# Kernel tuning notes

Hardware: AMD Instinct MI355X
Metric: run time of the kernel (lower is better)

The kernel has to match this reference:

```python
import jax, jax.numpy as jnp
import numpy as np

D_MODEL = 2048
N_HEADS = 16
N_KV_HEADS = 4
D_K = D_MODEL // N_HEADS  # 128
N_REP = N_HEADS // N_KV_HEADS
WINDOW = 128  # current_window_size default
RMS_EPS = 1e-8
ROPE_BASE = 10000.0
MASK_FILL = -10000.0


def _rmsnorm(x, w):
    rms = jnp.sqrt(jnp.mean(x * x, axis=-1, keepdims=True) + RMS_EPS)
    return x / rms * w


def _rope(x, cos, sin):
    # x: [B, S, H, d_k]; cos/sin: [S, d_k//2]; pairs are interleaved (..., -1, 2)
    B, S, H, dk = x.shape
    xr = x.reshape(B, S, H, dk // 2, 2)
    x1, x2 = xr[..., 0], xr[..., 1]
    c = cos[None, :, None, :]
    s = sin[None, :, None, :]
    o1 = x1 * c - x2 * s
    o2 = x1 * s + x2 * c
    return jnp.stack([o1, o2], axis=-1).reshape(B, S, H, dk)


def setup_inputs() -> dict:
    key = jax.random.key(0)
    ks = jax.random.split(key, 10)
    B, S = 2, 2048
    std = 1.0 / np.sqrt(D_MODEL)
    inp = {
        "x": jax.random.normal(ks[0], (B, S, D_MODEL), dtype=jnp.float32),
        "Wq": jax.random.normal(ks[1], (D_MODEL, D_MODEL), dtype=jnp.float32) * std,
        "bq": jnp.zeros((D_MODEL,), dtype=jnp.float32),
        "Wk": jax.random.normal(ks[2], (N_KV_HEADS * D_K, D_MODEL), dtype=jnp.float32) * std,
        "bk": jnp.zeros((N_KV_HEADS * D_K,), dtype=jnp.float32),
        "Wv": jax.random.normal(ks[3], (N_KV_HEADS * D_K, D_MODEL), dtype=jnp.float32) * std,
        "bv": jnp.zeros((N_KV_HEADS * D_K,), dtype=jnp.float32),
        "Wo": jax.random.normal(ks[4], (D_MODEL, D_MODEL), dtype=jnp.float32) * std,
        "bo": jnp.zeros((D_MODEL,), dtype=jnp.float32),
        "qn_w": jnp.ones((D_K,), dtype=jnp.float32),
        "kn_w": jnp.ones((D_K,), dtype=jnp.float32),
        "scale": jnp.asarray(1.0 / np.sqrt(D_K), dtype=jnp.float32),
    }
    return inp


def reference(x, Wq, bq, Wk, bk, Wv, bv, Wo, bo, qn_w, kn_w, scale):
    B, S, D = x.shape
    # projections
    q = (x @ Wq.T + bq).reshape(B, S, N_HEADS, D_K)
    k = (x @ Wk.T + bk).reshape(B, S, N_KV_HEADS, D_K)
    v = (x @ Wv.T + bv).reshape(B, S, N_KV_HEADS, D_K)
    # per-head RMSNorm
    q = _rmsnorm(q, qn_w)
    k = _rmsnorm(k, kn_w)
    # RoPE
    inv_freq = 1.0 / (ROPE_BASE ** (jnp.arange(0, D_K, 2, dtype=jnp.float32) / D_K))
    t = jnp.arange(S, dtype=jnp.float32)
    freqs = t[:, None] * inv_freq[None, :]  # [S, D_K//2]
    cos, sin = jnp.cos(freqs), jnp.sin(freqs)
    q = _rope(q, cos, sin)
    k = _rope(k, cos, sin)
    # [B, H, S, d_k]
    q = q.transpose(0, 2, 1, 3)
    k = k.transpose(0, 2, 1, 3)
    v = v.transpose(0, 2, 1, 3)
    # GQA repeat (repeat_interleave on head dim)
    k = jnp.repeat(k, N_REP, axis=1)
    v = jnp.repeat(v, N_REP, axis=1)
    # dense sliding-window path (window < seq_len)
    scores = jnp.einsum("bhqd,bhkd->bhqk", q, k) * scale
    idx = jnp.arange(S)
    causal = idx[:, None] < idx[None, :]  # triu diag=1
    local = jnp.abs(idx[:, None] - idx[None, :]) > (WINDOW // 2)
    mask = causal | local
    scores = jnp.where(mask[None, None, :, :], MASK_FILL, scores)
    attn = jax.nn.softmax(scores, axis=-1)
    out = jnp.einsum("bhqk,bhkd->bhqd", attn, v)
    out = out.transpose(0, 2, 1, 3).reshape(B, S, D)
    return out @ Wo.T + bo
```

## Files before the change

### kernel.cpp

```cpp
#include <hip/hip_runtime.h>

#define BATCH 2
#define SEQ 2048
#define DMODEL 2048
#define NHEADS 16
#define NKV 4
#define DK 128
#define WINH 64
#define NQKV 3072

typedef unsigned short ushort_t;
typedef __attribute__((ext_vector_type(8))) __bf16 bf16x8;
typedef __attribute__((ext_vector_type(4))) float f32x4;

__device__ __forceinline__ float b2f(ushort_t u) {
    union { unsigned int i; float f; } v; v.i = ((unsigned int)u) << 16; return v.f;
}
__device__ __forceinline__ ushort_t f2b(float f) {
    union { float f; unsigned int i; } v; v.f = f;
    unsigned int r = v.i + 0x7FFFu + ((v.i >> 16) & 1u);
    return (ushort_t)(r >> 16);
}

__device__ __forceinline__ void gload_lds16(const ushort_t* g, ushort_t* l) {
    __builtin_amdgcn_global_load_lds(
        (__attribute__((address_space(1))) void*)(void*)const_cast<ushort_t*>(g),
        (__attribute__((address_space(3))) void*)l, 16, 0, 0);
}

__global__ __launch_bounds__(256) void cvt_bf16(
    const float* __restrict__ src, ushort_t* __restrict__ dst, int n8)
{
    int i = blockIdx.x * 256 + threadIdx.x;
    if (i >= n8) return;
    float4 a = *((const float4*)src + i * 2);
    float4 b = *((const float4*)src + i * 2 + 1);
    ushort_t o[8] = { f2b(a.x), f2b(a.y), f2b(a.z), f2b(a.w),
                      f2b(b.x), f2b(b.y), f2b(b.z), f2b(b.w) };
    *((uint4*)dst + i) = *(const uint4*)o;
}

__global__ __launch_bounds__(256) void cvt_weights(
    const float* __restrict__ Wq, const float* __restrict__ Wk,
    const float* __restrict__ Wv, const float* __restrict__ Wo,
    ushort_t* __restrict__ dst)
{
    int i = blockIdx.x * 256 + threadIdx.x;
    int row = i >> 8;
    int c8  = i & 255;
    const float* src;
    if      (row < 2048) src = Wq + (size_t)row * 2048;
    else if (row < 2560) src = Wk + (size_t)(row - 2048) * 2048;
    else if (row < 3072) src = Wv + (size_t)(row - 2560) * 2048;
    else                 src = Wo + (size_t)(row - 3072) * 2048;
    float4 a = *((const float4*)src + c8 * 2);
    float4 b = *((const float4*)src + c8 * 2 + 1);
    ushort_t o[8] = { f2b(a.x), f2b(a.y), f2b(a.z), f2b(a.w),
                      f2b(b.x), f2b(b.y), f2b(b.z), f2b(b.w) };
    *((uint4*)dst + i) = *(const uint4*)o;
}

__global__ __launch_bounds__(256) void concat_bias3(
    const float* __restrict__ bq, const float* __restrict__ bk,
    const float* __restrict__ bv, float* __restrict__ dst)
{
    int i = blockIdx.x * 256 + threadIdx.x;
    if (i < 2048) dst[i] = bq[i];
    else if (i < 2560) dst[i] = bk[i - 2048];
    else if (i < 3072) dst[i] = bv[i - 2560];
}

__global__ __launch_bounds__(256) void gemm_qkv(
    const ushort_t* __restrict__ A, const ushort_t* __restrict__ W,
    const float* __restrict__ bias, ushort_t* __restrict__ C,
    int M, int N, int K)
{
    __shared__ __attribute__((aligned(16))) ushort_t sA[8192];
    __shared__ __attribute__((aligned(16))) ushort_t sB[8192];

    const int tid  = threadIdx.x;
    const int lane = tid & 63;
    const int wave = tid >> 6;
    const int nbn  = N >> 7;

    int nwg = gridDim.x;
    int bid = blockIdx.x;
    int nb  = (nwg & 7) ? bid : ((bid & 7) * (nwg >> 3) + (bid >> 3));
    const int bm = nb / nbn;
    const int bn = nb % nbn;
    const int m0 = bm << 7, n0 = bn << 7;
    const int wm = wave >> 1, wn = wave & 1;

    f32x4 acc[4][4] = {};

    const int frow = lane & 15;
    const int kg   = lane >> 4;

    const ushort_t* gA[4]; const ushort_t* gB[4];
    ushort_t* lA[4]; ushort_t* lB[4];
#pragma unroll
    for (int j = 0; j < 4; ++j) {
        int t = wave * 4 + j;
        int c = t * 64 + lane;
        int r = c >> 3, s = c & 7;
        int ksrc = s ^ (r & 7);
        gA[j] = A + (size_t)(m0 + r) * K + ksrc * 8;
        gB[j] = W + (size_t)(n0 + r) * K + ksrc * 8;
        lA[j] = sA + t * 512;
        lB[j] = sB + t * 512;
    }

    for (int k0 = 0; k0 < K; k0 += 64) {
        if (k0) __syncthreads();
#pragma unroll
        for (int j = 0; j < 4; ++j) gload_lds16(gA[j] + k0, lA[j]);
#pragma unroll
        for (int j = 0; j < 4; ++j) gload_lds16(gB[j] + k0, lB[j]);
        __syncthreads();

        bf16x8 af[4][2], bfr[4][2];
#pragma unroll
        for (int mi = 0; mi < 4; ++mi)
#pragma unroll
            for (int kk = 0; kk < 2; ++kk) {
                int r = (wm << 6) + (mi << 4) + frow;
                int sl = (kk * 4 + kg) ^ (r & 7);
                af[mi][kk] = *(const bf16x8*)(sA + (r * 8 + sl) * 8);
            }
#pragma unroll
        for (int ni = 0; ni < 4; ++ni)
#pragma unroll
            for (int kk = 0; kk < 2; ++kk) {
                int r = (wn << 6) + (ni << 4) + frow;
                int sl = (kk * 4 + kg) ^ (r & 7);
                bfr[ni][kk] = *(const bf16x8*)(sB + (r * 8 + sl) * 8);
            }
#pragma unroll
        for (int kk = 0; kk < 2; ++kk)
#pragma unroll
            for (int mi = 0; mi < 4; ++mi)
#pragma unroll
                for (int ni = 0; ni < 4; ++ni)
                    acc[mi][ni] = __builtin_amdgcn_mfma_f32_16x16x32_bf16(
                        af[mi][kk], bfr[ni][kk], acc[mi][ni], 0, 0, 0);
    }

    const int orow = (lane >> 4) << 2;
    const int ocol = lane & 15;
#pragma unroll
    for (int ni = 0; ni < 4; ++ni) {
        int col = n0 + (wn << 6) + (ni << 4) + ocol;
        float bvf = bias[col];
#pragma unroll
        for (int mi = 0; mi < 4; ++mi) {
#pragma unroll
            for (int r = 0; r < 4; ++r) {
                int row = m0 + (wm << 6) + (mi << 4) + orow + r;
                C[(size_t)row * N + col] = f2b(acc[mi][ni][r] + bvf);
            }
        }
    }
}

__global__ __launch_bounds__(128) void rmsrope(
    ushort_t* __restrict__ qkv, const float* __restrict__ qw,
    const float* __restrict__ kw)
{
    const int d   = threadIdx.x;
    const int blk = blockIdx.x;
    const int bs  = blk / 20;
    const int hh  = blk % 20;
    const int s   = bs & 2047;

    ushort_t* p = qkv + (size_t)bs * NQKV + hh * DK;
    const float* w = (hh < NHEADS) ? qw : kw;

    float x  = b2f(p[d]);
    float ss = x * x;
#pragma unroll
    for (int off = 32; off; off >>= 1) ss += __shfl_xor(ss, off, 64);
    float s2 = __shfl_xor(ss, 0, 64);
    __shared__ float red[2];
    if ((d & 63) == 0) red[d >> 6] = ss;
    __syncthreads();
    float tot = red[0] + red[1];
    (void)s2;
    float inv = rsqrtf(tot * (1.0f / 128.0f) + 1e-8f);
    float xn  = x * inv * w[d];

    float partner = __shfl_xor(xn, 1, 64);
    float invfreq = exp2f(-(float)(d & ~1) * (13.287712379549449f / 128.0f));
    float angle   = (float)s * invfreq;
    float c = cosf(angle), sn = sinf(angle);
    float o = (d & 1) ? (partner * sn + xn * c) : (xn * c - partner * sn);
    p[d] = f2b(o);
}

__global__ __launch_bounds__(512) void gemm_out_ks(
    const ushort_t* __restrict__ A, const ushort_t* __restrict__ W,
    const float* __restrict__ bias, float* __restrict__ C,
    int M, int N, int K)
{
    __shared__ __attribute__((aligned(16))) unsigned char smem[65536];
    ushort_t* sA = (ushort_t*)smem;
    ushort_t* sB = (ushort_t*)(smem + 16384);
    float*    red = (float*)smem;

    const int tid  = threadIdx.x;
    const int lane = tid & 63;
    const int wave = tid >> 6;
    const int g    = wave >> 2;
    const int q    = wave & 3;
    const int wm   = q >> 1, wn = q & 1;
    const int nbn  = N >> 7;

    int nwg = gridDim.x;
    int bid = blockIdx.x;
    int nb  = (nwg & 7) ? bid : ((bid & 7) * (nwg >> 3) + (bid >> 3));
    const int bm = nb / nbn;
    const int bn = nb % nbn;
    const int m0 = bm << 7, n0 = bn << 7;

    f32x4 acc[4][4] = {};

    const int frow = lane & 15;
    const int kg   = lane >> 4;

    const ushort_t* gA[2]; const ushort_t* gB[2];
    ushort_t* lA[2]; ushort_t* lB[2];
#pragma unroll
    for (int j = 0; j < 2; ++j) {
        int t = wave * 2 + j;
        int c = t * 64 + lane;
        int r = c >> 3, s = c & 7;
        int ksrc = s ^ (r & 7);
        gA[j] = A + (size_t)(m0 + r) * K + ksrc * 8;
        gB[j] = W + (size_t)(n0 + r) * K + ksrc * 8;
        lA[j] = sA + t * 512;
        lB[j] = sB + t * 512;
    }

    for (int k0 = 0; k0 < K; k0 += 64) {
        if (k0) __syncthreads();
#pragma unroll
        for (int j = 0; j < 2; ++j) gload_lds16(gA[j] + k0, lA[j]);
#pragma unroll
        for (int j = 0; j < 2; ++j) gload_lds16(gB[j] + k0, lB[j]);
        __syncthreads();

        bf16x8 af[4], bfr[4];
#pragma unroll
        for (int mi = 0; mi < 4; ++mi) {
            int r = (wm << 6) + (mi << 4) + frow;
            int sl = ((g << 2) + kg) ^ (r & 7);
            af[mi] = *(const bf16x8*)(sA + (r * 8 + sl) * 8);
        }
#pragma unroll
        for (int ni = 0; ni < 4; ++ni) {
            int r = (wn << 6) + (ni << 4) + frow;
            int sl = ((g << 2) + kg) ^ (r & 7);
            bfr[ni] = *(const bf16x8*)(sB + (r * 8 + sl) * 8);
        }
#pragma unroll
        for (int mi = 0; mi < 4; ++mi)
#pragma unroll
            for (int ni = 0; ni < 4; ++ni)
                acc[mi][ni] = __builtin_amdgcn_mfma_f32_16x16x32_bf16(
                    af[mi], bfr[ni], acc[mi][ni], 0, 0, 0);
    }

    __syncthreads();
    if (g == 1) {
#pragma unroll
        for (int mi = 0; mi < 4; ++mi)
#pragma unroll
            for (int ni = 0; ni < 4; ++ni)
                *(f32x4*)(red + q * 4096 + (mi * 4 + ni) * 256 + lane * 4) =
                    acc[mi][ni];
    }
    __syncthreads();

    if (g == 0) {
        const int orow = (lane >> 4) << 2;
        const int ocol = lane & 15;
#pragma unroll
        for (int ni = 0; ni < 4; ++ni) {
            int col = n0 + (wn << 6) + (ni << 4) + ocol;
            float bvf = bias[col];
#pragma unroll
            for (int mi = 0; mi < 4; ++mi) {
                f32x4 other = *(const f32x4*)(red + q * 4096 + (mi * 4 + ni) * 256 + lane * 4);
#pragma unroll
                for (int r = 0; r < 4; ++r) {
                    int row = m0 + (wm << 6) + (mi << 4) + orow + r;
                    C[(size_t)row * N + col] = acc[mi][ni][r] + other[r] + bvf;
                }
            }
        }
    }
}

__global__ __launch_bounds__(256) void attn_mfma(
    const ushort_t* __restrict__ qkv, const float* __restrict__ scp,
    ushort_t* __restrict__ ao)
{
    __shared__ __attribute__((aligned(16))) ushort_t sK[16384];
    __shared__ __attribute__((aligned(16))) ushort_t sVT[16384];

    const int tid  = threadIdx.x;
    const int lane = tid & 63;
    const int w    = tid >> 6;
    const int c    = lane & 15;
    const int g    = lane >> 4;

    const int blk = blockIdx.x;
    const int qt  = blk & 31;
    const int h   = (blk >> 5) & 15;
    const int b   = blk >> 9;
    const int kvh = h >> 2;
    const int i0  = qt << 6;
    const int jb  = i0 - 64;
    const float scale = scp[0];

    bf16x8 aq[4];
    {
        const ushort_t* qp = qkv + ((size_t)(b * 2048 + i0 + w * 16 + c)) * NQKV
                                 + h * 128 + g * 8;
#pragma unroll
        for (int ks = 0; ks < 4; ++ks)
            aq[ks] = *(const bf16x8*)(qp + ks * 32);
    }

    const ushort_t* kvb = qkv + ((size_t)b * 2048) * NQKV + 2048 + kvh * 128;
#pragma unroll
    for (int it = 0; it < 8; ++it) {
        int idx = it * 256 + tid;
        int rr = idx >> 4, cc = idx & 15;
        int j = jb + rr; if (j < 0) j = 0;
        uint4 val = *(const uint4*)(kvb + (size_t)j * NQKV + cc * 8);
        int f2v = (rr & 15) ^ ((rr >> 3) & 15);
        *(uint4*)(sK + (rr * 16 + (cc ^ f2v)) * 8) = val;
    }
#pragma unroll
    for (int it = 0; it < 4; ++it) {
        int task = it * 256 + tid;
        int pp = task >> 4, d8 = task & 15;
        int j0 = jb + 2 * pp;     if (j0 < 0) j0 = 0;
        int j1 = jb + 2 * pp + 1; if (j1 < 0) j1 = 0;
        ushort_t e0[8]; *(uint4*)e0 = *(const uint4*)(kvb + (size_t)j0 * NQKV + 512 + d8 * 8);
        ushort_t e1[8]; *(uint4*)e1 = *(const uint4*)(kvb + (size_t)j1 * NQKV + 512 + d8 * 8);
        int cc = pp >> 2;
#pragma unroll
        for (int jj = 0; jj < 8; ++jj) {
            int rr = d8 * 8 + jj;
            int f2v = (rr & 15) ^ ((rr >> 3) & 15);
            unsigned int word = (unsigned int)e0[jj] | ((unsigned int)e1[jj] << 16);
            *(unsigned int*)(sVT + (rr * 16 + (cc ^ f2v)) * 8 + (pp & 3) * 2) = word;
        }
    }
    __syncthreads();

    f32x4 s[8] = {};
#pragma unroll
    for (int nt = 0; nt < 8; ++nt) {
        int rr = nt * 16 + c;
        int f2v = (rr & 15) ^ ((rr >> 3) & 15);
#pragma unroll
        for (int ks = 0; ks < 4; ++ks) {
            bf16x8 bk = *(const bf16x8*)(sK + (rr * 16 + ((ks * 4 + g) ^ f2v)) * 8);
            s[nt] = __builtin_amdgcn_mfma_f32_16x16x32_bf16(aq[ks], bk, s[nt], 0, 0, 0);
        }
    }

    float linv[4];
#pragma unroll
    for (int r = 0; r < 4; ++r) {
        int qb = w * 16 + g * 4 + r;
#pragma unroll
        for (int nt = 0; nt < 8; ++nt) {
            int jl = nt * 16 + c;
            bool valid = (jl >= qb) && (jl <= qb + 64) && (i0 + jl >= 64);
            s[nt][r] = valid ? s[nt][r] * scale : -1e30f;
        }
        float m = s[0][r];
#pragma unroll
        for (int nt = 1; nt < 8; ++nt) m = fmaxf(m, s[nt][r]);
#pragma unroll
        for (int off = 1; off <= 8; off <<= 1) m = fmaxf(m, __shfl_xor(m, off, 64));
        float sum = 0.f;
#pragma unroll
        for (int nt = 0; nt < 8; ++nt) {
            float e = __expf(s[nt][r] - m);
            s[nt][r] = e;
            sum += e;
        }
#pragma unroll
        for (int off = 1; off <= 8; off <<= 1) sum += __shfl_xor(sum, off, 64);
        linv[r] = 1.0f / sum;
    }

    __syncthreads();
    float* Pw = (float*)sK + w * 2048;
#pragma unroll
    for (int nt = 0; nt < 8; ++nt) {
#pragma unroll
        for (int r = 0; r < 4; ++r) {
            int q = g * 4 + r;
            int chunk = nt * 4 + (c >> 2);
            Pw[q * 128 + ((chunk ^ (q & 7)) * 4) + (c & 3)] = s[nt][r];
        }
    }

    f32x4 o[8] = {};
#pragma unroll
    for (int kt = 0; kt < 4; ++kt) {
        float pf[8];
#pragma unroll
        for (int e = 0; e < 2; ++e) {
            int chunk = kt * 8 + g * 2 + e;
            f32x4 v4 = *(const f32x4*)(Pw + c * 128 + ((chunk ^ (c & 7)) * 4));
            pf[e * 4 + 0] = v4[0]; pf[e * 4 + 1] = v4[1];
            pf[e * 4 + 2] = v4[2]; pf[e * 4 + 3] = v4[3];
        }
        ushort_t pb[8];
#pragma unroll
        for (int j = 0; j < 8; ++j) pb[j] = f2b(pf[j]);
        bf16x8 pa = *(const bf16x8*)pb;
#pragma unroll
        for (int dt = 0; dt < 8; ++dt) {
            int rr = dt * 16 + c;
            int f2v = (rr & 15) ^ ((rr >> 3) & 15);
            bf16x8 bv = *(const bf16x8*)(sVT + (rr * 16 + ((kt * 4 + g) ^ f2v)) * 8);
            o[dt] = __builtin_amdgcn_mfma_f32_16x16x32_bf16(pa, bv, o[dt], 0, 0, 0);
        }
    }

    const size_t orow0 = (size_t)(b * 2048 + i0 + w * 16);
#pragma unroll
    for (int dt = 0; dt < 8; ++dt) {
#pragma unroll
        for (int r = 0; r < 4; ++r) {
            int q = g * 4 + r;
            ao[(orow0 + q) * 2048 + h * 128 + dt * 16 + c] = f2b(o[dt][r] * linv[r]);
        }
    }
}

extern "C" void kernel_launch(void* const* d_in, const int* in_sizes, int n_in,
                              void* d_out, int out_size, void* d_ws, size_t ws_size,
                              hipStream_t stream)
{
    const float* x   = (const float*)d_in[0];
    const float* Wq  = (const float*)d_in[1];
    const float* bq  = (const float*)d_in[2];
    const float* Wk  = (const float*)d_in[3];
    const float* bk  = (const float*)d_in[4];
    const float* Wv  = (const float*)d_in[5];
    const float* bv  = (const float*)d_in[6];
    const float* Wo  = (const float*)d_in[7];
    const float* bo  = (const float*)d_in[8];
    const float* qnw = (const float*)d_in[9];
    const float* knw = (const float*)d_in[10];
    const float* scp = (const float*)d_in[11];
    float* out = (float*)d_out;

    const int M = BATCH * SEQ;
    ushort_t* xb    = (ushort_t*)d_ws;
    ushort_t* qkv0  = xb   + (size_t)M * DMODEL;
    ushort_t* Wqkvb = qkv0 + (size_t)M * NQKV;
    ushort_t* Wob   = Wqkvb + (size_t)NQKV * DMODEL;
    float*    bqkv  = (float*)(Wob + (size_t)DMODEL * DMODEL);
    ushort_t* ao    = xb;
    (void)ws_size; (void)in_sizes; (void)n_in; (void)out_size;

    cvt_bf16<<<dim3(4096), 256, 0, stream>>>(x, xb, M * DMODEL / 8);
    cvt_weights<<<dim3(5120), 256, 0, stream>>>(Wq, Wk, Wv, Wo, Wqkvb);
    concat_bias3<<<dim3(12), 256, 0, stream>>>(bq, bk, bv, bqkv);

    gemm_qkv<<<dim3((M / 128) * (NQKV / 128)), 256, 0, stream>>>(
        xb, Wqkvb, bqkv, qkv0, M, NQKV, DMODEL);
    rmsrope<<<dim3(M * (NHEADS + NKV)), 128, 0, stream>>>(qkv0, qnw, knw);
    attn_mfma<<<dim3(BATCH * NHEADS * (SEQ / 64)), 256, 0, stream>>>(qkv0, scp, ao);
    gemm_out_ks<<<dim3((M / 128) * (DMODEL / 128)), 512, 0, stream>>>(
        ao, Wob, bo, out, M, DMODEL, DMODEL);
}
```

Measured before the change: 164.5 us.

## Fuse RMSNorm+RoPE into attention loads and merge prep kernels

Removes the standalone rmsrope kernel. Per-head RMSNorm and RoPE are now applied to Q and K as they are loaded inside the attention kernel, using a cos/sin table that is precomputed once per call. The softmax scale is folded into the Q normalisation factor. The three conversion/bias kernels are merged into one prep launch that also builds the rope table. This cuts launches and a full read-modify-write pass over qkv, at the cost of recomputing K normalisation in each query-tile block that shares the same K rows.

```diff
diff --git a/kernel.cpp b/kernel.cpp
--- a/kernel.cpp
+++ b/kernel.cpp
@@ -28,46 +28,48 @@
         (__attribute__((address_space(3))) void*)l, 16, 0, 0);
 }
 
-__global__ __launch_bounds__(256) void cvt_bf16(
-    const float* __restrict__ src, ushort_t* __restrict__ dst, int n8)
+__global__ __launch_bounds__(256) void prep(
+    const float* __restrict__ x,  const float* __restrict__ Wq,
+    const float* __restrict__ Wk, const float* __restrict__ Wv,
+    const float* __restrict__ Wo, const float* __restrict__ bq,
+    const float* __restrict__ bk, const float* __restrict__ bv,
+    ushort_t* __restrict__ xb, ushort_t* __restrict__ wdst,
+    float* __restrict__ bqkv, float2* __restrict__ rtab)
 {
-    int i = blockIdx.x * 256 + threadIdx.x;
-    if (i >= n8) return;
-    float4 a = *((const float4*)src + i * 2);
-    float4 b = *((const float4*)src + i * 2 + 1);
-    ushort_t o[8] = { f2b(a.x), f2b(a.y), f2b(a.z), f2b(a.w),
-                      f2b(b.x), f2b(b.y), f2b(b.z), f2b(b.w) };
-    *((uint4*)dst + i) = *(const uint4*)o;
-}
-
-__global__ __launch_bounds__(256) void cvt_weights(
-    const float* __restrict__ Wq, const float* __restrict__ Wk,
-    const float* __restrict__ Wv, const float* __restrict__ Wo,
-    ushort_t* __restrict__ dst)
-{
-    int i = blockIdx.x * 256 + threadIdx.x;
-    int row = i >> 8;
-    int c8  = i & 255;
-    const float* src;
-    if      (row < 2048) src = Wq + (size_t)row * 2048;
-    else if (row < 2560) src = Wk + (size_t)(row - 2048) * 2048;
-    else if (row < 3072) src = Wv + (size_t)(row - 2560) * 2048;
-    else                 src = Wo + (size_t)(row - 3072) * 2048;
-    float4 a = *((const float4*)src + c8 * 2);
-    float4 b = *((const float4*)src + c8 * 2 + 1);
-    ushort_t o[8] = { f2b(a.x), f2b(a.y), f2b(a.z), f2b(a.w),
-                      f2b(b.x), f2b(b.y), f2b(b.z), f2b(b.w) };
-    *((uint4*)dst + i) = *(const uint4*)o;
-}
-
-__global__ __launch_bounds__(256) void concat_bias3(
-    const float* __restrict__ bq, const float* __restrict__ bk,
-    const float* __restrict__ bv, float* __restrict__ dst)
-{
-    int i = blockIdx.x * 256 + threadIdx.x;
-    if (i < 2048) dst[i] = bq[i];
-    else if (i < 2560) dst[i] = bk[i - 2048];
-    else if (i < 3072) dst[i] = bv[i - 2560];
+    const int blk = blockIdx.x;
+    const int tid = threadIdx.x;
+    if (blk < 4096) {
+        int i = blk * 256 + tid;
+        float4 a = *((const float4*)x + i * 2);
+        float4 b = *((const float4*)x + i * 2 + 1);
+        ushort_t o[8] = { f2b(a.x), f2b(a.y), f2b(a.z), f2b(a.w),
+                          f2b(b.x), f2b(b.y), f2b(b.z), f2b(b.w) };
+        *((uint4*)xb + i) = *(const uint4*)o;
+    } else if (blk < 9216) {
+        int i = (blk - 4096) * 256 + tid;
+        int row = i >> 8, c8 = i & 255;
+        const float* src;
+        if      (row < 2048) src = Wq + (size_t)row * 2048;
+        else if (row < 2560) src = Wk + (size_t)(row - 2048) * 2048;
+        else if (row < 3072) src = Wv + (size_t)(row - 2560) * 2048;
+        else                 src = Wo + (size_t)(row - 3072) * 2048;
+        float4 a = *((const float4*)src + c8 * 2);
+        float4 b = *((const float4*)src + c8 * 2 + 1);
+        ushort_t o[8] = { f2b(a.x), f2b(a.y), f2b(a.z), f2b(a.w),
+                          f2b(b.x), f2b(b.y), f2b(b.z), f2b(b.w) };
+        *((uint4*)wdst + i) = *(const uint4*)o;
+    } else if (blk < 9228) {
+        int i = (blk - 9216) * 256 + tid;
+        if (i < 2048) bqkv[i] = bq[i];
+        else if (i < 2560) bqkv[i] = bk[i - 2048];
+        else if (i < 3072) bqkv[i] = bv[i - 2560];
+    } else {
+        int i = (blk - 9228) * 256 + tid;
+        int s = i >> 6, dd = i & 63;
+        float invfreq = exp2f(-(float)(2 * dd) * (13.287712379549449f / 128.0f));
+        float ang = (float)s * invfreq;
+        rtab[i] = make_float2(cosf(ang), sinf(ang));
+    }
 }
 
 __global__ __launch_bounds__(256) void gemm_qkv(
@@ -162,40 +164,6 @@
     }
 }
 
-__global__ __launch_bounds__(128) void rmsrope(
-    ushort_t* __restrict__ qkv, const float* __restrict__ qw,
-    const float* __restrict__ kw)
-{
-    const int d   = threadIdx.x;
-    const int blk = blockIdx.x;
-    const int bs  = blk / 20;
-    const int hh  = blk % 20;
-    const int s   = bs & 2047;
-
-    ushort_t* p = qkv + (size_t)bs * NQKV + hh * DK;
-    const float* w = (hh < NHEADS) ? qw : kw;
-
-    float x  = b2f(p[d]);
-    float ss = x * x;
-#pragma unroll
-    for (int off = 32; off; off >>= 1) ss += __shfl_xor(ss, off, 64);
-    float s2 = __shfl_xor(ss, 0, 64);
-    __shared__ float red[2];
-    if ((d & 63) == 0) red[d >> 6] = ss;
-    __syncthreads();
-    float tot = red[0] + red[1];
-    (void)s2;
-    float inv = rsqrtf(tot * (1.0f / 128.0f) + 1e-8f);
-    float xn  = x * inv * w[d];
-
-    float partner = __shfl_xor(xn, 1, 64);
-    float invfreq = exp2f(-(float)(d & ~1) * (13.287712379549449f / 128.0f));
-    float angle   = (float)s * invfreq;
-    float c = cosf(angle), sn = sinf(angle);
-    float o = (d & 1) ? (partner * sn + xn * c) : (xn * c - partner * sn);
-    p[d] = f2b(o);
-}
-
 __global__ __launch_bounds__(512) void gemm_out_ks(
     const ushort_t* __restrict__ A, const ushort_t* __restrict__ W,
     const float* __restrict__ bias, float* __restrict__ C,
@@ -301,8 +269,9 @@
 }
 
 __global__ __launch_bounds__(256) void attn_mfma(
-    const ushort_t* __restrict__ qkv, const float* __restrict__ scp,
-    ushort_t* __restrict__ ao)
+    const ushort_t* __restrict__ qkv, const float* __restrict__ qn_w,
+    const float* __restrict__ kn_w, const float* __restrict__ scp,
+    const float2* __restrict__ rtab, ushort_t* __restrict__ ao)
 {
     __shared__ __attribute__((aligned(16))) ushort_t sK[16384];
     __shared__ __attribute__((aligned(16))) ushort_t sVT[16384];
@@ -324,11 +293,40 @@
 
     bf16x8 aq[4];
     {
-        const ushort_t* qp = qkv + ((size_t)(b * 2048 + i0 + w * 16 + c)) * NQKV
+        const int srow = i0 + w * 16 + c;
+        const ushort_t* qp = qkv + ((size_t)(b * 2048 + srow)) * NQKV
                                  + h * 128 + g * 8;
-#pragma unroll
-        for (int ks = 0; ks < 4; ++ks)
-            aq[ks] = *(const bf16x8*)(qp + ks * 32);
+        float xv[4][8];
+        float ss = 0.f;
+#pragma unroll
+        for (int ks = 0; ks < 4; ++ks) {
+            ushort_t raw[8];
+            *(uint4*)raw = *(const uint4*)(qp + ks * 32);
+#pragma unroll
+            for (int j = 0; j < 8; ++j) {
+                float xf = b2f(raw[j]);
+                xv[ks][j] = xf;
+                ss += xf * xf;
+            }
+        }
+        ss += __shfl_xor(ss, 16, 64);
+        ss += __shfl_xor(ss, 32, 64);
+        float inv = rsqrtf(ss * (1.0f / 128.0f) + 1e-8f) * scale;
+#pragma unroll
+        for (int ks = 0; ks < 4; ++ks) {
+            ushort_t outb[8];
+#pragma unroll
+            for (int jj = 0; jj < 4; ++jj) {
+                int d = ks * 32 + g * 8 + 2 * jj;
+                float2 w2 = *(const float2*)(qn_w + d);
+                float x0 = xv[ks][2 * jj]     * inv * w2.x;
+                float x1 = xv[ks][2 * jj + 1] * inv * w2.y;
+                float2 cs = rtab[(srow << 6) + (d >> 1)];
+                outb[2 * jj]     = f2b(x0 * cs.x - x1 * cs.y);
+                outb[2 * jj + 1] = f2b(x0 * cs.y + x1 * cs.x);
+            }
+            aq[ks] = *(const bf16x8*)outb;
+        }
     }
 
     const ushort_t* kvb = qkv + ((size_t)b * 2048) * NQKV + 2048 + kvh * 128;
@@ -337,9 +335,33 @@
         int idx = it * 256 + tid;
         int rr = idx >> 4, cc = idx & 15;
         int j = jb + rr; if (j < 0) j = 0;
-        uint4 val = *(const uint4*)(kvb + (size_t)j * NQKV + cc * 8);
+        ushort_t raw[8];
+        *(uint4*)raw = *(const uint4*)(kvb + (size_t)j * NQKV + cc * 8);
+        float xv[8];
+        float ss = 0.f;
+#pragma unroll
+        for (int jj = 0; jj < 8; ++jj) {
+            xv[jj] = b2f(raw[jj]);
+            ss += xv[jj] * xv[jj];
+        }
+        ss += __shfl_xor(ss, 1, 64);
+        ss += __shfl_xor(ss, 2, 64);
+        ss += __shfl_xor(ss, 4, 64);
+        ss += __shfl_xor(ss, 8, 64);
+        float inv = rsqrtf(ss * (1.0f / 128.0f) + 1e-8f);
+        ushort_t outb[8];
+#pragma unroll
+        for (int jj = 0; jj < 4; ++jj) {
+            int d = cc * 8 + 2 * jj;
+            float2 w2 = *(const float2*)(kn_w + d);
+            float x0 = xv[2 * jj]     * inv * w2.x;
+            float x1 = xv[2 * jj + 1] * inv * w2.y;
+            float2 cs = rtab[(j << 6) + (d >> 1)];
+            outb[2 * jj]     = f2b(x0 * cs.x - x1 * cs.y);
+            outb[2 * jj + 1] = f2b(x0 * cs.y + x1 * cs.x);
+        }
         int f2v = (rr & 15) ^ ((rr >> 3) & 15);
-        *(uint4*)(sK + (rr * 16 + (cc ^ f2v)) * 8) = val;
+        *(uint4*)(sK + (rr * 16 + (cc ^ f2v)) * 8) = *(const uint4*)outb;
     }
 #pragma unroll
     for (int it = 0; it < 4; ++it) {
@@ -380,7 +402,7 @@
         for (int nt = 0; nt < 8; ++nt) {
             int jl = nt * 16 + c;
             bool valid = (jl >= qb) && (jl <= qb + 64) && (i0 + jl >= 64);
-            s[nt][r] = valid ? s[nt][r] * scale : -1e30f;
+            s[nt][r] = valid ? s[nt][r] : -1e30f;
         }
         float m = s[0][r];
 #pragma unroll
@@ -470,17 +492,16 @@
     ushort_t* Wqkvb = qkv0 + (size_t)M * NQKV;
     ushort_t* Wob   = Wqkvb + (size_t)NQKV * DMODEL;
     float*    bqkv  = (float*)(Wob + (size_t)DMODEL * DMODEL);
+    float2*   rtab  = (float2*)(bqkv + 3072);
     ushort_t* ao    = xb;
     (void)ws_size; (void)in_sizes; (void)n_in; (void)out_size;
 
-    cvt_bf16<<<dim3(4096), 256, 0, stream>>>(x, xb, M * DMODEL / 8);
-    cvt_weights<<<dim3(5120), 256, 0, stream>>>(Wq, Wk, Wv, Wo, Wqkvb);
-    concat_bias3<<<dim3(12), 256, 0, stream>>>(bq, bk, bv, bqkv);
-
+    prep<<<dim3(9740), 256, 0, stream>>>(x, Wq, Wk, Wv, Wo, bq, bk, bv,
+                                         xb, Wqkvb, bqkv, rtab);
     gemm_qkv<<<dim3((M / 128) * (NQKV / 128)), 256, 0, stream>>>(
         xb, Wqkvb, bqkv, qkv0, M, NQKV, DMODEL);
-    rmsrope<<<dim3(M * (NHEADS + NKV)), 128, 0, stream>>>(qkv0, qnw, knw);
-    attn_mfma<<<dim3(BATCH * NHEADS * (SEQ / 64)), 256, 0, stream>>>(qkv0, scp, ao);
+    attn_mfma<<<dim3(BATCH * NHEADS * (SEQ / 64)), 256, 0, stream>>>(
+        qkv0, qnw, knw, scp, rtab, ao);
     gemm_out_ks<<<dim3((M / 128) * (DMODEL / 128)), 512, 0, stream>>>(
         ao, Wob, bo, out, M, DMODEL, DMODEL);
 }
```

New measurement: 139.7 us. 15.1% less time.
